# Kernel tuning notes

Measured on AMD Instinct MI355X. Metric: run time of the kernel, lower is better.

Reference implementation:

```python
import jax, jax.numpy as jnp
import numpy as np

N = 50000   # nodes
E = 800000  # edges
D = 200     # h_dim == out_dim
R = 500     # num_rels
L = 2       # num_hidden_layers
RRELU_SLOPE = (1.0 / 8.0 + 1.0 / 3.0) / 2.0  # eval-mode F.rrelu negative slope


def _rrelu(x):
    return jnp.where(x >= 0, x, x * jnp.float32(RRELU_SLOPE))


def setup_inputs() -> dict:
    key = jax.random.key(0)
    ks = jax.random.split(key, 10)
    s = np.float32(1.0 / np.sqrt(D))  # ~xavier scale
    return {
        "init_ent_emb": jax.random.normal(ks[0], (N, D), jnp.float32),
        "rel_emb": jax.random.normal(ks[1], (R, D), jnp.float32),
        "weight_neighbor": jax.random.normal(ks[2], (L, D, D), jnp.float32) * s,
        "loop_weight": jax.random.normal(ks[3], (L, D, D), jnp.float32) * s,
        "evolve_loop_weight": jax.random.normal(ks[4], (L, D, D), jnp.float32) * s,
        "norm": jax.random.uniform(ks[5], (N, 1), jnp.float32),
        "src": jax.random.randint(ks[6], (E,), 0, N, dtype=jnp.int32),
        "dst": jax.random.randint(ks[7], (E,), 0, N, dtype=jnp.int32),
        "etype": jax.random.randint(ks[8], (E,), 0, R, dtype=jnp.int32),
        "node_id": jnp.arange(N, dtype=jnp.int32),
    }


def reference(init_ent_emb, rel_emb, weight_neighbor, loop_weight,
              evolve_loop_weight, norm, src, dst, etype, node_id):
    # g.ndata['h'] = init_ent_emb[node_id]
    h = init_ent_emb[node_id]                                    # [N, D]
    # mask of nodes with in-degree > 0 (fixed across layers)
    indeg = jnp.zeros((N,), jnp.float32).at[dst].add(1.0)
    has_in = (indeg > 0)[:, None]                                # [N, 1]
    for l in range(L):
        # loop message: loop_weight where in-degree>0, evolve_loop_weight otherwise
        loop_msg = jnp.where(has_in,
                             h @ loop_weight[l],
                             h @ evolve_loop_weight[l])          # [N, D]
        # per-edge message: (h_src + rel_emb[etype]) @ W_neighbor
        msg = (h[src] + rel_emb[etype]) @ weight_neighbor[l]     # [E, D]
        # sum-scatter to destination nodes, then per-node norm (apply_func)
        agg = jax.ops.segment_sum(msg, dst, num_segments=N)      # [N, D]
        h = _rrelu(agg * norm + loop_msg)
    return h
```

## Files before the change

kernel.cpp:

```cpp
#include <hip/hip_runtime.h>

#define D 200
#define RRELU_SLOPE 0.22916666666666666f
#define STRIDE 96
#define PAD 8

typedef unsigned short u16;
typedef unsigned int u32;

using bf16x8 = __attribute__((ext_vector_type(8))) short;
using f32x4  = __attribute__((ext_vector_type(4))) float;
using f32x2  = __attribute__((ext_vector_type(2))) float;

__device__ __forceinline__ float rrelu(float x) {
    return x >= 0.0f ? x : x * RRELU_SLOPE;
}
__device__ __forceinline__ float bf2f(u32 u) {
    union { u32 i; float f; } c; c.i = u << 16; return c.f;
}
__device__ __forceinline__ u32 f2bf(float f) {
    union { float f; u32 i; } c; c.f = f;
    return (c.i + 0x7fffu + ((c.i >> 16) & 1u)) >> 16;
}
__device__ __forceinline__ u32 pack2(float x, float y) {
    return f2bf(x) | (f2bf(y) << 16);
}
__device__ __forceinline__ void gll16(const void* g, void* l) {
    __builtin_amdgcn_global_load_lds((const __attribute__((address_space(1))) void*)g,
                                     (__attribute__((address_space(3))) void*)l,
                                     16, 0, 0);
}

__device__ __forceinline__ void accw(u32 w, f32x2& acc) {
    union { u32 i; float f; } lo, hi;
    lo.i = w << 16;
    hi.i = w & 0xffff0000u;
    f32x2 t; t[0] = lo.f; t[1] = hi.f;
    acc += t;
}
__device__ __forceinline__ void accq(uint4 q, f32x2* a) {
    accw(q.x, a[0]); accw(q.y, a[1]); accw(q.z, a[2]); accw(q.w, a[3]);
}


__global__ void prep_k(const float* __restrict__ rel, const float* __restrict__ Wn,
                       const float* __restrict__ Wl, u16* __restrict__ relb,
                       u16* __restrict__ Bt, u16* __restrict__ hb0d,
                       u16* __restrict__ hb1d, int* __restrict__ noin_cnt) {
    int i = blockIdx.x * blockDim.x + threadIdx.x;
    if (i == 0) *noin_cnt = 0;
    if (i < 200) { hb0d[i] = 0; hb1d[i] = 0; }
    if (i < 100200) relb[i] = (i < 100000) ? (u16)f2bf(rel[i]) : (u16)0;
    if (i < 2 * 256 * 416) {
        int l = i / (256 * 416);
        int rem = i % (256 * 416);
        int c = rem / 416;
        int k = rem % 416;
        float v = 0.0f;
        if (c < 200 && k < 400)
            v = (k < 200) ? Wn[(size_t)l * 40000 + k * 200 + c]
                          : Wl[(size_t)l * 40000 + (k - 200) * 200 + c];
        Bt[i] = (u16)f2bf(v);
    }
}


__global__ void scatter_k(const int* __restrict__ dst, const int* __restrict__ src,
                          const int* __restrict__ etype, int* __restrict__ cnt,
                          u32* __restrict__ ep, int E) {
    int e = blockIdx.x * blockDim.x + threadIdx.x;
    if (e < E) {
        int d = dst[e];
        int c = atomicAdd(&cnt[d], 1);
        if (c < STRIDE)
            ep[(size_t)d * STRIDE + c] = (u32)src[e] | ((u32)etype[e] << 17);
    }
}

__global__ void pad_k(const int* __restrict__ cnt, u32* __restrict__ ep, u32 dummy,
                      int* __restrict__ noin, int* __restrict__ noin_cnt, int N) {
    int v = blockIdx.x * blockDim.x + threadIdx.x;
    if (v >= N) return;
    int c = cnt[v];
    if (c == 0) noin[atomicAdd(noin_cnt, 1)] = v;
    int e = (c + PAD - 1) & ~(PAD - 1);
    for (int i = c; i < e; ++i) ep[(size_t)v * STRIDE + i] = dummy;
}


__global__ void gather_k(const float* __restrict__ init, const int* __restrict__ nid,
                         u16* __restrict__ hb, int N) {
    int lane = threadIdx.x & 63;
    int v = blockIdx.x * 4 + (threadIdx.x >> 6);
    if (v >= N || lane >= 50) return;
    float4 f = *(const float4*)(init + (size_t)nid[v] * D + lane * 4);
    uint2 o;
    o.x = pack2(f.x, f.y);
    o.y = pack2(f.z, f.w);
    *(uint2*)(hb + (size_t)v * D + lane * 4) = o;
}


__global__ __launch_bounds__(256) void gagg0_k(
        const u16* __restrict__ hb, const u16* __restrict__ relb,
        const u32* __restrict__ ep, const int* __restrict__ cnt,
        const float* __restrict__ norm,
        u16* __restrict__ aggb, u16* __restrict__ relsumb, int N, u32 dummy) {
    int lane = threadIdx.x & 63;
    int wave = threadIdx.x >> 6;
    int li = lane & 31;
    int v = blockIdx.x * 8 + wave * 2 + (lane >> 5);
    if (v >= N || li >= 25) return;
    size_t lo = (size_t)li * 8;
    const u16* hbL = hb + lo;
    const u16* rbL = relb + lo;
    int c = cnt[v];
    if (c > STRIDE) c = STRIDE;
    int rv = (c + PAD - 1) >> 3;
    const u32* pp = ep + (size_t)v * STRIDE;
    f32x2 a[4] = {}, rr[4] = {};
    u32 p[8];
    uint4 qh[8];
#pragma unroll
    for (int j = 0; j < 8; ++j) p[j] = (rv > 0) ? pp[j] : dummy;
#pragma unroll
    for (int j = 0; j < 8; ++j)
        qh[j] = *(const uint4*)(hbL + (size_t)(p[j] & 0x1FFFFu) * D);
    for (int r = 0; r < rv; ++r) {
        u32 pn[8];
#pragma unroll
        for (int j = 0; j < 8; ++j)
            pn[j] = (r + 1 < rv) ? pp[(size_t)(r + 1) * 8 + j] : dummy;
        uint4 qr[8];
#pragma unroll
        for (int j = 0; j < 8; ++j)
            qr[j] = *(const uint4*)(rbL + (size_t)((p[j] >> 17) & 0x3FFu) * D);
#pragma unroll
        for (int j = 0; j < 8; ++j) accq(qh[j], a);
#pragma unroll
        for (int j = 0; j < 8; ++j)
            qh[j] = *(const uint4*)(hbL + (size_t)(pn[j] & 0x1FFFFu) * D);
#pragma unroll
        for (int j = 0; j < 8; ++j) accq(qr[j], rr);
#pragma unroll
        for (int j = 0; j < 8; ++j) p[j] = pn[j];
    }
    uint4 rs;
    rs.x = pack2(rr[0][0], rr[0][1]); rs.y = pack2(rr[1][0], rr[1][1]);
    rs.z = pack2(rr[2][0], rr[2][1]); rs.w = pack2(rr[3][0], rr[3][1]);
    *(uint4*)(relsumb + (size_t)v * D + lo) = rs;
    float nv = norm[v];
    uint4 o;
    o.x = pack2((a[0][0] + rr[0][0]) * nv, (a[0][1] + rr[0][1]) * nv);
    o.y = pack2((a[1][0] + rr[1][0]) * nv, (a[1][1] + rr[1][1]) * nv);
    o.z = pack2((a[2][0] + rr[2][0]) * nv, (a[2][1] + rr[2][1]) * nv);
    o.w = pack2((a[3][0] + rr[3][0]) * nv, (a[3][1] + rr[3][1]) * nv);
    *(uint4*)(aggb + (size_t)v * D + lo) = o;
}


__global__ __launch_bounds__(256) void gagg1_k(
        const u16* __restrict__ hb, const u32* __restrict__ ep,
        const int* __restrict__ cnt, const float* __restrict__ norm,
        const u16* __restrict__ addb, u16* __restrict__ outb, int N, u32 dummy) {
    int lane = threadIdx.x & 63;
    int wave = threadIdx.x >> 6;
    int li = lane & 31;
    int v = blockIdx.x * 8 + wave * 2 + (lane >> 5);
    if (v >= N || li >= 25) return;
    size_t lo = (size_t)li * 8;
    const u16* hbL = hb + lo;
    int c = cnt[v];
    if (c > STRIDE) c = STRIDE;
    int rv = (c + PAD - 1) >> 3;
    const u32* pp = ep + (size_t)v * STRIDE;
    f32x2 a[4] = {};
    u32 p[8];
    uint4 qh[8];
#pragma unroll
    for (int j = 0; j < 8; ++j) p[j] = (rv > 0) ? pp[j] : dummy;
#pragma unroll
    for (int j = 0; j < 8; ++j)
        qh[j] = *(const uint4*)(hbL + (size_t)(p[j] & 0x1FFFFu) * D);
    for (int r = 0; r < rv; ++r) {
        u32 pn[8];
#pragma unroll
        for (int j = 0; j < 8; ++j)
            pn[j] = (r + 1 < rv) ? pp[(size_t)(r + 1) * 8 + j] : dummy;
#pragma unroll
        for (int j = 0; j < 8; ++j) accq(qh[j], a);
#pragma unroll
        for (int j = 0; j < 8; ++j)
            qh[j] = *(const uint4*)(hbL + (size_t)(pn[j] & 0x1FFFFu) * D);
#pragma unroll
        for (int j = 0; j < 8; ++j) p[j] = pn[j];
    }
    {
        uint4 q = *(const uint4*)(addb + (size_t)v * D + lo);
        accq(q, a);
    }
    float nv = norm[v];
    uint4 o;
    o.x = pack2(a[0][0] * nv, a[0][1] * nv);
    o.y = pack2(a[1][0] * nv, a[1][1] * nv);
    o.z = pack2(a[2][0] * nv, a[2][1] * nv);
    o.w = pack2(a[3][0] * nv, a[3][1] * nv);
    *(uint4*)(outb + (size_t)v * D + lo) = o;
}


__global__ __launch_bounds__(256) void gemm_k(
        const u16* __restrict__ Aagg, const u16* __restrict__ Ah,
        const u16* __restrict__ Bt,
        float* __restrict__ outF, u16* __restrict__ outB, int M) {
    __shared__ __align__(16) u16 As[64 * 32];
    __shared__ __align__(16) u16 Bs[256 * 32];
    int tid = threadIdx.x;
    int lane = tid & 63;
    int wave = tid >> 6;
    int rowBase = blockIdx.x * 64;
    int m = lane & 15;
    int kq = (lane >> 4) * 8;

    int srow = tid >> 2;
    int kg = (tid & 3) * 8;

    u16* ldsA = As + (size_t)wave * 512;

    f32x4 acc[4][4] = {};

    for (int k0 = 0; k0 < 416; k0 += 32) {
        int k = k0 + kg;
        {
            const u16* gA = (k < 200) ? Aagg + (size_t)(rowBase + srow) * D + k
                                      : Ah + (size_t)(rowBase + srow) * D + (k - 200);
            gll16(gA, ldsA);
#pragma unroll
            for (int p = 0; p < 4; ++p) {
                const u16* gB = Bt + (size_t)(p * 64 + srow) * 416 + k;
                gll16(gB, Bs + ((size_t)p * 2048 + wave * 512));
            }
        }
        __syncthreads();

        bf16x8 a0 = *(const bf16x8*)(As + (m) * 32 + kq);
        bf16x8 a1 = *(const bf16x8*)(As + (16 + m) * 32 + kq);
        bf16x8 a2 = *(const bf16x8*)(As + (32 + m) * 32 + kq);
        bf16x8 a3 = *(const bf16x8*)(As + (48 + m) * 32 + kq);
        int wc = wave * 64;
        bf16x8 b0 = *(const bf16x8*)(Bs + (wc + m) * 32 + kq);
        bf16x8 b1 = *(const bf16x8*)(Bs + (wc + 16 + m) * 32 + kq);
        bf16x8 b2 = *(const bf16x8*)(Bs + (wc + 32 + m) * 32 + kq);
        bf16x8 b3 = *(const bf16x8*)(Bs + (wc + 48 + m) * 32 + kq);
        acc[0][0] = __builtin_amdgcn_mfma_f32_16x16x32_bf16(a0, b0, acc[0][0], 0, 0, 0);
        acc[0][1] = __builtin_amdgcn_mfma_f32_16x16x32_bf16(a0, b1, acc[0][1], 0, 0, 0);
        acc[0][2] = __builtin_amdgcn_mfma_f32_16x16x32_bf16(a0, b2, acc[0][2], 0, 0, 0);
        acc[0][3] = __builtin_amdgcn_mfma_f32_16x16x32_bf16(a0, b3, acc[0][3], 0, 0, 0);
        acc[1][0] = __builtin_amdgcn_mfma_f32_16x16x32_bf16(a1, b0, acc[1][0], 0, 0, 0);
        acc[1][1] = __builtin_amdgcn_mfma_f32_16x16x32_bf16(a1, b1, acc[1][1], 0, 0, 0);
        acc[1][2] = __builtin_amdgcn_mfma_f32_16x16x32_bf16(a1, b2, acc[1][2], 0, 0, 0);
        acc[1][3] = __builtin_amdgcn_mfma_f32_16x16x32_bf16(a1, b3, acc[1][3], 0, 0, 0);
        acc[2][0] = __builtin_amdgcn_mfma_f32_16x16x32_bf16(a2, b0, acc[2][0], 0, 0, 0);
        acc[2][1] = __builtin_amdgcn_mfma_f32_16x16x32_bf16(a2, b1, acc[2][1], 0, 0, 0);
        acc[2][2] = __builtin_amdgcn_mfma_f32_16x16x32_bf16(a2, b2, acc[2][2], 0, 0, 0);
        acc[2][3] = __builtin_amdgcn_mfma_f32_16x16x32_bf16(a2, b3, acc[2][3], 0, 0, 0);
        acc[3][0] = __builtin_amdgcn_mfma_f32_16x16x32_bf16(a3, b0, acc[3][0], 0, 0, 0);
        acc[3][1] = __builtin_amdgcn_mfma_f32_16x16x32_bf16(a3, b1, acc[3][1], 0, 0, 0);
        acc[3][2] = __builtin_amdgcn_mfma_f32_16x16x32_bf16(a3, b2, acc[3][2], 0, 0, 0);
        acc[3][3] = __builtin_amdgcn_mfma_f32_16x16x32_bf16(a3, b3, acc[3][3], 0, 0, 0);
        __syncthreads();
    }

    int cRow = (lane >> 4) * 4;
    int cCol = lane & 15;
#pragma unroll
    for (int i = 0; i < 4; ++i) {
#pragma unroll
        for (int j = 0; j < 4; ++j) {
            int col = wave * 64 + j * 16 + cCol;
            if (col >= 200) continue;
#pragma unroll
            for (int r = 0; r < 4; ++r) {
                int row = rowBase + i * 16 + cRow + r;
                if (row < M) {
                    float val = rrelu(acc[i][j][r]);
                    if (outF) outF[(size_t)row * D + col] = val;
                    if (outB) outB[(size_t)row * D + col] = (u16)f2bf(val);
                }
            }
        }
    }
}


__global__ void fixup_k(const u16* __restrict__ hb, const float* __restrict__ We,
                        const int* __restrict__ noin, const int* __restrict__ noin_cnt,
                        float* __restrict__ outF, u16* __restrict__ outB) {
    int cnt = *noin_cnt;
    for (int i = blockIdx.x; i < cnt; i += gridDim.x) {
        int v = noin[i];
        int j = threadIdx.x;
        if (j < D) {
            float acc = 0.0f;
            for (int k = 0; k < D; ++k)
                acc += bf2f(hb[(size_t)v * D + k]) * We[(size_t)k * D + j];
            float r = rrelu(acc);
            if (outF) outF[(size_t)v * D + j] = r;
            if (outB) outB[(size_t)v * D + j] = (u16)f2bf(r);
        }
    }
}

extern "C" void kernel_launch(void* const* d_in, const int* in_sizes, int n_in,
                              void* d_out, int out_size, void* d_ws, size_t ws_size,
                              hipStream_t stream) {
    const float* init  = (const float*)d_in[0];
    const float* rel   = (const float*)d_in[1];
    const float* Wn    = (const float*)d_in[2];
    const float* Wl    = (const float*)d_in[3];
    const float* We    = (const float*)d_in[4];
    const float* norm  = (const float*)d_in[5];
    const int* src     = (const int*)d_in[6];
    const int* dst     = (const int*)d_in[7];
    const int* etype   = (const int*)d_in[8];
    const int* node_id = (const int*)d_in[9];
    float* out = (float*)d_out;

    int N = in_sizes[5];
    int E = in_sizes[6];
    size_t NP = (size_t)N + 256;

    char* w = (char*)d_ws;
    auto carve = [&](size_t bytes) {
        char* p = w;
        w += (bytes + 255) & ~(size_t)255;
        return p;
    };
    u16* hb0     = (u16*)carve(NP * D * sizeof(u16));
    u16* hb1     = (u16*)carve(NP * D * sizeof(u16));
    u16* aggb    = (u16*)carve(NP * D * sizeof(u16));
    u16* relsumb = (u16*)carve((size_t)N * D * sizeof(u16));
    u16* relb    = (u16*)carve((size_t)501 * D * sizeof(u16));
    u16* Bt      = (u16*)carve((size_t)2 * 256 * 416 * sizeof(u16));
    int* cnt     = (int*)carve((size_t)N * sizeof(int));
    u32* epack   = (u32*)carve(((size_t)N * STRIDE + PAD) * sizeof(u32));
    int* noin    = (int*)carve((size_t)N * sizeof(int));
    int* noin_cnt = (int*)carve(sizeof(int));

    (void)hipMemsetAsync(cnt, 0, (size_t)N * sizeof(int), stream);

    int prepN = 2 * 256 * 416;
    prep_k<<<(prepN + 255) / 256, 256, 0, stream>>>(rel, Wn, Wl, relb, Bt,
                                                    hb0 + (size_t)N * D,
                                                    hb1 + (size_t)N * D, noin_cnt);
    scatter_k<<<(E + 255) / 256, 256, 0, stream>>>(dst, src, etype, cnt, epack, E);
    u32 dummy = (u32)N | (500u << 17);
    pad_k<<<(N + 255) / 256, 256, 0, stream>>>(cnt, epack, dummy, noin, noin_cnt, N);
    gather_k<<<(N + 3) / 4, 256, 0, stream>>>(init, node_id, hb0, N);

    int gemmBlocks = (N + 63) / 64;

    gagg0_k<<<(N + 7) / 8, 256, 0, stream>>>(hb0, relb, epack, cnt, norm,
                                             aggb, relsumb, N, dummy);
    gemm_k<<<gemmBlocks, 256, 0, stream>>>(aggb, hb0, Bt, nullptr, hb1, N);
    fixup_k<<<8, 256, 0, stream>>>(hb0, We, noin, noin_cnt, nullptr, hb1);

    gagg1_k<<<(N + 7) / 8, 256, 0, stream>>>(hb1, epack, cnt, norm,
                                             relsumb, aggb, N, dummy);
    gemm_k<<<gemmBlocks, 256, 0, stream>>>(aggb, hb1, Bt + 256 * 416, out, nullptr, N);
    fixup_k<<<8, 256, 0, stream>>>(hb1, We + D * D, noin, noin_cnt, out, nullptr);
}
```

Measured before the change: 358.0 us.

## Merge prep, scatter and gather kernels; double-buffer GEMM LDS tiles

Three independent front-end kernels (weight/rel conversion, edge scatter, node-embedding gather) are merged into one launch that dispatches by block index, removing two launch gaps and letting their work run concurrently. The GEMM kernel now double-buffers its A/B LDS tiles, issuing the global-to-LDS loads for the next K step before computing the current one, so there is one barrier per step instead of two. The cost is doubled LDS per block (about 40KB), which may reduce occupancy. Correctness of the overlap depends on the asynchronous LDS loads being complete before the barrier that precedes their use.

```diff
diff --git a/kernel.cpp b/kernel.cpp
--- a/kernel.cpp
+++ b/kernel.cpp
@@ -43,37 +43,50 @@
 }
 
 
-__global__ void prep_k(const float* __restrict__ rel, const float* __restrict__ Wn,
-                       const float* __restrict__ Wl, u16* __restrict__ relb,
-                       u16* __restrict__ Bt, u16* __restrict__ hb0d,
-                       u16* __restrict__ hb1d, int* __restrict__ noin_cnt) {
-    int i = blockIdx.x * blockDim.x + threadIdx.x;
-    if (i == 0) *noin_cnt = 0;
-    if (i < 200) { hb0d[i] = 0; hb1d[i] = 0; }
-    if (i < 100200) relb[i] = (i < 100000) ? (u16)f2bf(rel[i]) : (u16)0;
-    if (i < 2 * 256 * 416) {
-        int l = i / (256 * 416);
-        int rem = i % (256 * 416);
-        int c = rem / 416;
-        int k = rem % 416;
-        float v = 0.0f;
-        if (c < 200 && k < 400)
-            v = (k < 200) ? Wn[(size_t)l * 40000 + k * 200 + c]
-                          : Wl[(size_t)l * 40000 + (k - 200) * 200 + c];
-        Bt[i] = (u16)f2bf(v);
-    }
-}
-
-
-__global__ void scatter_k(const int* __restrict__ dst, const int* __restrict__ src,
-                          const int* __restrict__ etype, int* __restrict__ cnt,
-                          u32* __restrict__ ep, int E) {
-    int e = blockIdx.x * blockDim.x + threadIdx.x;
-    if (e < E) {
-        int d = dst[e];
-        int c = atomicAdd(&cnt[d], 1);
-        if (c < STRIDE)
-            ep[(size_t)d * STRIDE + c] = (u32)src[e] | ((u32)etype[e] << 17);
+__global__ void front_k(const float* __restrict__ rel, const float* __restrict__ Wn,
+                        const float* __restrict__ Wl, u16* __restrict__ relb,
+                        u16* __restrict__ Bt, u16* __restrict__ hb0d,
+                        u16* __restrict__ hb1d, int* __restrict__ noin_cnt,
+                        const int* __restrict__ dst, const int* __restrict__ src,
+                        const int* __restrict__ etype, int* __restrict__ cnt,
+                        u32* __restrict__ ep, int E,
+                        const float* __restrict__ init, const int* __restrict__ nid,
+                        u16* __restrict__ hb, int N,
+                        int prepB, int scatB) {
+    int b = blockIdx.x;
+    if (b < prepB) {
+        int i = b * blockDim.x + threadIdx.x;
+        if (i == 0) *noin_cnt = 0;
+        if (i < 200) { hb0d[i] = 0; hb1d[i] = 0; }
+        if (i < 100200) relb[i] = (i < 100000) ? (u16)f2bf(rel[i]) : (u16)0;
+        if (i < 2 * 256 * 416) {
+            int l = i / (256 * 416);
+            int rem = i % (256 * 416);
+            int c = rem / 416;
+            int k = rem % 416;
+            float v = 0.0f;
+            if (c < 200 && k < 400)
+                v = (k < 200) ? Wn[(size_t)l * 40000 + k * 200 + c]
+                              : Wl[(size_t)l * 40000 + (k - 200) * 200 + c];
+            Bt[i] = (u16)f2bf(v);
+        }
+    } else if (b < prepB + scatB) {
+        int e = (b - prepB) * blockDim.x + threadIdx.x;
+        if (e < E) {
+            int d = dst[e];
+            int c = atomicAdd(&cnt[d], 1);
+            if (c < STRIDE)
+                ep[(size_t)d * STRIDE + c] = (u32)src[e] | ((u32)etype[e] << 17);
+        }
+    } else {
+        int lane = threadIdx.x & 63;
+        int v = (b - prepB - scatB) * 4 + (threadIdx.x >> 6);
+        if (v >= N || lane >= 50) return;
+        float4 f = *(const float4*)(init + (size_t)nid[v] * D + lane * 4);
+        uint2 o;
+        o.x = pack2(f.x, f.y);
+        o.y = pack2(f.z, f.w);
+        *(uint2*)(hb + (size_t)v * D + lane * 4) = o;
     }
 }
 
@@ -85,19 +98,6 @@
     if (c == 0) noin[atomicAdd(noin_cnt, 1)] = v;
     int e = (c + PAD - 1) & ~(PAD - 1);
     for (int i = c; i < e; ++i) ep[(size_t)v * STRIDE + i] = dummy;
-}
-
-
-__global__ void gather_k(const float* __restrict__ init, const int* __restrict__ nid,
-                         u16* __restrict__ hb, int N) {
-    int lane = threadIdx.x & 63;
-    int v = blockIdx.x * 4 + (threadIdx.x >> 6);
-    if (v >= N || lane >= 50) return;
-    float4 f = *(const float4*)(init + (size_t)nid[v] * D + lane * 4);
-    uint2 o;
-    o.x = pack2(f.x, f.y);
-    o.y = pack2(f.z, f.w);
-    *(uint2*)(hb + (size_t)v * D + lane * 4) = o;
 }
 
 
@@ -213,8 +213,8 @@
         const u16* __restrict__ Aagg, const u16* __restrict__ Ah,
         const u16* __restrict__ Bt,
         float* __restrict__ outF, u16* __restrict__ outB, int M) {
-    __shared__ __align__(16) u16 As[64 * 32];
-    __shared__ __align__(16) u16 Bs[256 * 32];
+    __shared__ __align__(16) u16 As[2][64 * 32];
+    __shared__ __align__(16) u16 Bs[2][256 * 32];
     int tid = threadIdx.x;
     int lane = tid & 63;
     int wave = tid >> 6;
@@ -224,34 +224,40 @@
 
     int srow = tid >> 2;
     int kg = (tid & 3) * 8;
-
-    u16* ldsA = As + (size_t)wave * 512;
+    size_t aRow = (size_t)(rowBase + srow);
 
     f32x4 acc[4][4] = {};
 
-    for (int k0 = 0; k0 < 416; k0 += 32) {
+    auto stage = [&](int buf, int k0) {
         int k = k0 + kg;
-        {
-            const u16* gA = (k < 200) ? Aagg + (size_t)(rowBase + srow) * D + k
-                                      : Ah + (size_t)(rowBase + srow) * D + (k - 200);
-            gll16(gA, ldsA);
-#pragma unroll
-            for (int p = 0; p < 4; ++p) {
-                const u16* gB = Bt + (size_t)(p * 64 + srow) * 416 + k;
-                gll16(gB, Bs + ((size_t)p * 2048 + wave * 512));
-            }
-        }
-        __syncthreads();
-
-        bf16x8 a0 = *(const bf16x8*)(As + (m) * 32 + kq);
-        bf16x8 a1 = *(const bf16x8*)(As + (16 + m) * 32 + kq);
-        bf16x8 a2 = *(const bf16x8*)(As + (32 + m) * 32 + kq);
-        bf16x8 a3 = *(const bf16x8*)(As + (48 + m) * 32 + kq);
+        const u16* gA = (k < 200) ? Aagg + aRow * D + k
+                                  : Ah + aRow * D + (k - 200);
+        gll16(gA, &As[buf][0] + wave * 512);
+#pragma unroll
+        for (int p = 0; p < 4; ++p) {
+            const u16* gB = Bt + (size_t)(p * 64 + srow) * 416 + k;
+            gll16(gB, &Bs[buf][0] + p * 2048 + wave * 512);
+        }
+    };
+
+    stage(0, 0);
+    __syncthreads();
+
+    int cur = 0;
+    for (int t = 0; t < 13; ++t) {
+        if (t < 12) stage(cur ^ 1, (t + 1) * 32);
+
+        const u16* A = &As[cur][0];
+        const u16* B = &Bs[cur][0];
+        bf16x8 a0 = *(const bf16x8*)(A + (m) * 32 + kq);
+        bf16x8 a1 = *(const bf16x8*)(A + (16 + m) * 32 + kq);
+        bf16x8 a2 = *(const bf16x8*)(A + (32 + m) * 32 + kq);
+        bf16x8 a3 = *(const bf16x8*)(A + (48 + m) * 32 + kq);
         int wc = wave * 64;
-        bf16x8 b0 = *(const bf16x8*)(Bs + (wc + m) * 32 + kq);
-        bf16x8 b1 = *(const bf16x8*)(Bs + (wc + 16 + m) * 32 + kq);
-        bf16x8 b2 = *(const bf16x8*)(Bs + (wc + 32 + m) * 32 + kq);
-        bf16x8 b3 = *(const bf16x8*)(Bs + (wc + 48 + m) * 32 + kq);
+        bf16x8 b0 = *(const bf16x8*)(B + (wc + m) * 32 + kq);
+        bf16x8 b1 = *(const bf16x8*)(B + (wc + 16 + m) * 32 + kq);
+        bf16x8 b2 = *(const bf16x8*)(B + (wc + 32 + m) * 32 + kq);
+        bf16x8 b3 = *(const bf16x8*)(B + (wc + 48 + m) * 32 + kq);
         acc[0][0] = __builtin_amdgcn_mfma_f32_16x16x32_bf16(a0, b0, acc[0][0], 0, 0, 0);
         acc[0][1] = __builtin_amdgcn_mfma_f32_16x16x32_bf16(a0, b1, acc[0][1], 0, 0, 0);
         acc[0][2] = __builtin_amdgcn_mfma_f32_16x16x32_bf16(a0, b2, acc[0][2], 0, 0, 0);
@@ -268,7 +274,9 @@
         acc[3][1] = __builtin_amdgcn_mfma_f32_16x16x32_bf16(a3, b1, acc[3][1], 0, 0, 0);
         acc[3][2] = __builtin_amdgcn_mfma_f32_16x16x32_bf16(a3, b2, acc[3][2], 0, 0, 0);
         acc[3][3] = __builtin_amdgcn_mfma_f32_16x16x32_bf16(a3, b3, acc[3][3], 0, 0, 0);
+
         __syncthreads();
+        cur ^= 1;
     }
 
     int cRow = (lane >> 4) * 4;
@@ -350,13 +358,17 @@
     (void)hipMemsetAsync(cnt, 0, (size_t)N * sizeof(int), stream);
 
     int prepN = 2 * 256 * 416;
-    prep_k<<<(prepN + 255) / 256, 256, 0, stream>>>(rel, Wn, Wl, relb, Bt,
-                                                    hb0 + (size_t)N * D,
-                                                    hb1 + (size_t)N * D, noin_cnt);
-    scatter_k<<<(E + 255) / 256, 256, 0, stream>>>(dst, src, etype, cnt, epack, E);
+    int prepB = (prepN + 255) / 256;
+    int scatB = (E + 255) / 256;
+    int gathB = (N + 3) / 4;
+    front_k<<<prepB + scatB + gathB, 256, 0, stream>>>(
+        rel, Wn, Wl, relb, Bt,
+        hb0 + (size_t)N * D, hb1 + (size_t)N * D, noin_cnt,
+        dst, src, etype, cnt, epack, E,
+        init, node_id, hb0, N, prepB, scatB);
+
     u32 dummy = (u32)N | (500u << 17);
     pad_k<<<(N + 255) / 256, 256, 0, stream>>>(cnt, epack, dummy, noin, noin_cnt, N);
-    gather_k<<<(N + 3) / 4, 256, 0, stream>>>(init, node_id, hb0, N);
 
     int gemmBlocks = (N + 63) / 64;
 
```

Result: faster. 350.2 us (-2.2%).
